# Optimization experiments

Hardware: AMD Instinct MI355X
Metric: run time of the kernel (lower is better)

Reference implementation:

```python
import jax, jax.numpy as jnp
import numpy as np

NUM_HEADS = 12
HEAD_SIZE = 64  # hidden 768 / 12 heads


def setup_inputs() -> dict:
    key = jax.random.key(0)
    ks = jax.random.split(key, 5)
    B, M, P, H = 8, 4, 512, 768
    scale = 1.0 / np.sqrt(H)
    return {
        "hidden_states": jax.random.normal(ks[0], (B, M, P, H), dtype=jnp.float32),
        "Wq": jax.random.normal(ks[1], (H, H), dtype=jnp.float32) * scale,
        "bq": jnp.zeros((H,), dtype=jnp.float32),
        "Wk": jax.random.normal(ks[2], (H, H), dtype=jnp.float32) * scale,
        "bk": jnp.zeros((H,), dtype=jnp.float32),
        "Wv": jax.random.normal(ks[3], (H, H), dtype=jnp.float32) * scale,
        "bv": jnp.zeros((H,), dtype=jnp.float32),
        "Wo": jax.random.normal(ks[4], (H, H), dtype=jnp.float32) * scale,
        "bo": jnp.zeros((H,), dtype=jnp.float32),
    }


def reference(hidden_states, Wq, bq, Wk, bk, Wv, bv, Wo, bo):
    # hidden_states: [B, M, P, H] (batch, modalities, patches, hidden)
    B, M, P, H = hidden_states.shape
    nh, hs = NUM_HEADS, HEAD_SIZE

    def split_heads(x):  # [B,M,P,H] -> [B,M,nh,P,hs]
        return x.reshape(B, M, P, nh, hs).transpose(0, 1, 3, 2, 4)

    q = split_heads(hidden_states @ Wq + bq)
    k = split_heads(hidden_states @ Wk + bk)
    v = split_heads(hidden_states @ Wv + bv)

    # per-modality, per-head attention over patches
    scores = jnp.einsum('bmnqh,bmnkh->bmnqk', q, k) / np.sqrt(hs).astype(jnp.float32)
    probs = jax.nn.softmax(scores, axis=-1)  # [B,M,nh,P,P]
    ctx = jnp.einsum('bmnqk,bmnkh->bmnqh', probs, v)
    ctx = ctx.transpose(0, 1, 3, 2, 4).reshape(B, M, P, H)  # merge heads

    # output projection (dropout rate 0.0 -> identity)
    return ctx @ Wo + bo
```

## Files before the change

kernel.cpp:

```cpp
#include <hip/hip_runtime.h>
#include <cstdint>
#include <cstddef>

#define H_DIM 768
#define NHEADS 12
#define HSZ 64
#define PATCH 512
#define MTOT 16384
#define SZT ((long)MTOT * H_DIM)

using short8 = __attribute__((ext_vector_type(8))) short;
using f32x4  = __attribute__((ext_vector_type(4))) float;
using us4    = __attribute__((ext_vector_type(4))) unsigned short;

#define GLL16(gp, lp) __builtin_amdgcn_global_load_lds( \
    (const __attribute__((address_space(1))) void*)(gp), \
    (__attribute__((address_space(3))) void*)(lp), 16, 0, 0)

__device__ __forceinline__ void split_f32(float x, unsigned short& h, unsigned short& l) {
    unsigned u = __float_as_uint(x);
    h = (unsigned short)(u >> 16);
    float rem = __uint_as_float(u & 0xffff0000u);
    float r = x - rem;
    unsigned v = __float_as_uint(r);
    v += 0x7fff + ((v >> 16) & 1);
    l = (unsigned short)(v >> 16);
}

__device__ __forceinline__ unsigned short bf16rne(float x) {
    unsigned v = __float_as_uint(x);
    v += 0x7fff + ((v >> 16) & 1);
    return (unsigned short)(v >> 16);
}

__global__ __launch_bounds__(256) void prep_x(const float* __restrict__ X,
                                              unsigned short* __restrict__ Xb)
{
    const long i = ((long)blockIdx.x * 256 + threadIdx.x) * 8;
    float4 a = *(const float4*)&X[i];
    float4 b = *(const float4*)&X[i + 4];
    float xs[8] = {a.x, a.y, a.z, a.w, b.x, b.y, b.z, b.w};
    us4 h0, h1;
    #pragma unroll
    for (int j = 0; j < 4; ++j) { h0[j] = bf16rne(xs[j]); h1[j] = bf16rne(xs[j + 4]); }
    *(us4*)&Xb[i] = h0; *(us4*)&Xb[i + 4] = h1;
}

template<int LO>
__global__ __launch_bounds__(256) void prep_w(const float* __restrict__ W,
                                              unsigned short* __restrict__ Whi,
                                              unsigned short* __restrict__ Wlo)
{
    __shared__ float T[64][65];
    const int kt = blockIdx.x * 64, nt = blockIdx.y * 64;
    const int tid = threadIdx.x;
    const int r = tid >> 2, c16 = (tid & 3) * 16;
    #pragma unroll
    for (int j = 0; j < 4; ++j) {
        float4 v = *(const float4*)&W[(long)(kt + r) * H_DIM + nt + c16 + j * 4];
        T[r][c16 + j*4 + 0] = v.x; T[r][c16 + j*4 + 1] = v.y;
        T[r][c16 + j*4 + 2] = v.z; T[r][c16 + j*4 + 3] = v.w;
    }
    __syncthreads();
    unsigned short* ph = &Whi[(long)(nt + r) * H_DIM + kt + c16];
    #pragma unroll
    for (int j = 0; j < 16; ++j) {
        if (LO) {
            unsigned short hh, ll;
            split_f32(T[c16 + j][r], hh, ll);
            ph[j] = hh;
            Wlo[(long)(nt + r) * H_DIM + kt + c16 + j] = ll;
        } else {
            ph[j] = bf16rne(T[c16 + j][r]);
        }
    }
}

__global__ __launch_bounds__(256, 4) void qkv_gemm(
    const unsigned short* __restrict__ Xb,
    const unsigned short* __restrict__ WqH, const unsigned short* __restrict__ WkH,
    const unsigned short* __restrict__ WvH,
    const float* __restrict__ bq, const float* __restrict__ bk, const float* __restrict__ bv,
    float qscale,
    unsigned short* __restrict__ Qt, unsigned short* __restrict__ Kp,
    unsigned short* __restrict__ Vp)
{
    __shared__ unsigned short As[8192];
    __shared__ unsigned short Bs[8192];

    const int s   = blockIdx.x + 18 * blockIdx.y;
    const int lid = (s & 7) * 288 + (s >> 3);
    const int bx  = lid % 18;
    const int by  = lid / 18;

    const int mat = bx / 6;
    const int n0  = (bx % 6) * 128;
    const int m0  = by * 128;
    const unsigned short* Bh = (mat == 0) ? WqH : (mat == 1) ? WkH : WvH;
    const float* bias        = (mat == 0) ? bq  : (mat == 1) ? bk  : bv;
    const float scale        = (mat == 0) ? qscale : 1.0f;

    const int tid  = threadIdx.x;
    const int lane = tid & 63;
    const int wv   = tid >> 6;
    const int wr   = wv >> 1, wc = wv & 1;
    const int q    = lane >> 4, l15 = lane & 15;

    const int srow   = tid >> 3;
    const int schunk = (tid & 7) ^ (srow & 7);

    char* ldsA = (char*)(&As[0]) + (wv << 10);
    char* ldsB = (char*)(&Bs[0]) + (wv << 10);

    f32x4 acc[4][4];
    #pragma unroll
    for (int i = 0; i < 4; ++i)
        #pragma unroll
        for (int j = 0; j < 4; ++j) acc[i][j] = 0;

    const int swz = (l15 & 7);

    for (int k0 = 0; k0 < H_DIM; k0 += 64) {
        #pragma unroll
        for (int i = 0; i < 4; ++i) {
            GLL16(Xb + (long)(m0 + i * 32 + srow) * H_DIM + k0 + schunk * 8,
                  ldsA + i * 4096);
            GLL16(Bh + (long)(n0 + i * 32 + srow) * H_DIM + k0 + schunk * 8,
                  ldsB + i * 4096);
        }
        __syncthreads();

        #pragma unroll
        for (int ks = 0; ks < 2; ++ks) {
            const int pc = ((ks * 4 + q) ^ swz) * 8;
            short8 ah[4], bh[4];
            #pragma unroll
            for (int t = 0; t < 4; ++t) {
                const int mr = wr * 64 + t * 16 + l15;
                ah[t] = *(const short8*)&As[mr * 64 + pc];
                const int nr = wc * 64 + t * 16 + l15;
                bh[t] = *(const short8*)&Bs[nr * 64 + pc];
            }
            #pragma unroll
            for (int mt = 0; mt < 4; ++mt)
                #pragma unroll
                for (int nt = 0; nt < 4; ++nt)
                    acc[mt][nt] = __builtin_amdgcn_mfma_f32_16x16x32_bf16(ah[mt], bh[nt], acc[mt][nt], 0, 0, 0);
        }
        __syncthreads();
    }

    #pragma unroll
    for (int nt = 0; nt < 4; ++nt) {
        const int col = n0 + wc * 64 + nt * 16 + l15;
        const float bcol = bias[col];
        const int h = col >> 6, d = col & 63;
        #pragma unroll
        for (int mt = 0; mt < 4; ++mt) {
            const int rowB = m0 + wr * 64 + mt * 16 + q * 4;
            #pragma unroll
            for (int r = 0; r < 4; ++r) {
                const int row = rowB + r;
                const float val = (acc[mt][nt][r] + bcol) * scale;
                const int bm = row >> 9, p = row & 511;
                const int bmh = bm * NHEADS + h;
                if (mat == 0) {
                    const long idx = ((long)bmh * 8 + (p >> 6)) * 4096 + (long)(p & 63) * 64 + d;
                    Qt[idx] = bf16rne(val);
                } else if (mat == 1) {
                    Kp[(long)bmh * 32768 + (long)p * 64 + d] = bf16rne(val);
                } else {
                    Vp[(long)bmh * 32768 + (long)d * 512 + p] = bf16rne(val);
                }
            }
        }
    }
}

__global__ __launch_bounds__(256, 4) void attn2(
    const unsigned short* __restrict__ Qt,
    const unsigned short* __restrict__ Kp, const unsigned short* __restrict__ Vp,
    unsigned short* __restrict__ Ctx)
{
    __shared__ unsigned short Ks[4096];
    __shared__ unsigned short Vs[4096];
    __shared__ unsigned short Ps[128 * 72];
    __shared__ float red[128][2];

    const int tid  = threadIdx.x;
    const int lane = tid & 63;
    const int wv   = tid >> 6;
    const int wr   = wv >> 1, wc = wv & 1;
    const int q    = lane >> 4, l15 = lane & 15;

    const int s   = blockIdx.x + 4 * blockIdx.y;
    const int lid = (s & 7) * 192 + (s >> 3);
    const int qt2 = lid & 3;
    const int bmh = lid >> 2;

    short8 qh[4][2];
    const long qtile = ((long)bmh * 8 + qt2 * 2 + wr) * 4096;
    #pragma unroll
    for (int mt = 0; mt < 4; ++mt)
        #pragma unroll
        for (int ks = 0; ks < 2; ++ks)
            qh[mt][ks] = *(const short8*)&Qt[qtile + (mt * 16 + l15) * 64 + ks * 32 + q * 8];

    f32x4 ctx[4][2];
    float l_cur[4][4];
    #pragma unroll
    for (int mt = 0; mt < 4; ++mt) {
        ctx[mt][0] = 0; ctx[mt][1] = 0;
        #pragma unroll
        for (int r = 0; r < 4; ++r) l_cur[mt][r] = 0.0f;
    }

    const long khead = (long)bmh * 32768;
    const int srow   = tid >> 3;
    const int gchunk = ((tid & 7) ^ (srow & 7)) * 8;
    char* dK = (char*)&Ks[0] + (wv << 10);
    char* dV = (char*)&Vs[0] + (wv << 10);

    for (int kt = 0; kt < 8; ++kt) {
        __syncthreads();
        {
            const long kb = khead + (long)kt * 64 * 64;
            GLL16(Kp + kb + (long)srow * 64 + gchunk,        dK);
            GLL16(Kp + kb + (long)(srow + 32) * 64 + gchunk, dK + 4096);
            const long vb = khead + (long)kt * 64;
            GLL16(Vp + vb + (long)srow * 512 + gchunk,        dV);
            GLL16(Vp + vb + (long)(srow + 32) * 512 + gchunk, dV + 4096);
        }
        __syncthreads();

        f32x4 s[4][2];
        #pragma unroll
        for (int mt = 0; mt < 4; ++mt) { s[mt][0] = 0; s[mt][1] = 0; }
        short8 kf[2][2];
        #pragma unroll
        for (int nt = 0; nt < 2; ++nt)
            #pragma unroll
            for (int ks = 0; ks < 2; ++ks) {
                const int key = wc * 32 + nt * 16 + l15;
                const int phys = (q + ks * 4) ^ (key & 7);
                kf[nt][ks] = *(const short8*)&Ks[key * 64 + phys * 8];
            }
        #pragma unroll
        for (int mt = 0; mt < 4; ++mt)
            #pragma unroll
            for (int nt = 0; nt < 2; ++nt)
                #pragma unroll
                for (int ks = 0; ks < 2; ++ks)
                    s[mt][nt] = __builtin_amdgcn_mfma_f32_16x16x32_bf16(qh[mt][ks], kf[nt][ks], s[mt][nt], 0, 0, 0);

        #pragma unroll
        for (int mt = 0; mt < 4; ++mt)
            #pragma unroll
            for (int r = 0; r < 4; ++r) {
                const int row = wr * 64 + mt * 16 + q * 4 + r;
                const float p0 = __builtin_amdgcn_exp2f(s[mt][0][r]);
                const float p1 = __builtin_amdgcn_exp2f(s[mt][1][r]);
                l_cur[mt][r] += p0 + p1;
                Ps[row * 72 + wc * 32 + l15]      = bf16rne(p0);
                Ps[row * 72 + wc * 32 + 16 + l15] = bf16rne(p1);
            }
        __syncthreads();

        short8 pf[4][2], vf[2][2];
        #pragma unroll
        for (int mt = 0; mt < 4; ++mt)
            #pragma unroll
            for (int ks = 0; ks < 2; ++ks)
                pf[mt][ks] = *(const short8*)&Ps[(wr * 64 + mt * 16 + l15) * 72 + ks * 32 + q * 8];
        #pragma unroll
        for (int nt = 0; nt < 2; ++nt)
            #pragma unroll
            for (int ks = 0; ks < 2; ++ks) {
                const int d = wc * 32 + nt * 16 + l15;
                const int phys = (q + ks * 4) ^ (d & 7);
                vf[nt][ks] = *(const short8*)&Vs[d * 64 + phys * 8];
            }
        #pragma unroll
        for (int mt = 0; mt < 4; ++mt)
            #pragma unroll
            for (int nt = 0; nt < 2; ++nt)
                #pragma unroll
                for (int ks = 0; ks < 2; ++ks)
                    ctx[mt][nt] = __builtin_amdgcn_mfma_f32_16x16x32_bf16(pf[mt][ks], vf[nt][ks], ctx[mt][nt], 0, 0, 0);
    }

    #pragma unroll
    for (int mt = 0; mt < 4; ++mt)
        #pragma unroll
        for (int r = 0; r < 4; ++r) {
            float v = l_cur[mt][r];
            v += __shfl_xor(v, 1);
            v += __shfl_xor(v, 2);
            v += __shfl_xor(v, 4);
            v += __shfl_xor(v, 8);
            if (l15 == 0) red[wr * 64 + mt * 16 + q * 4 + r][wc] = v;
        }
    __syncthreads();
    #pragma unroll
    for (int mt = 0; mt < 4; ++mt)
        #pragma unroll
        for (int r = 0; r < 4; ++r) {
            const int row = wr * 64 + mt * 16 + q * 4 + r;
            const float2 rd = *(const float2*)&red[row][0];
            const float inv = 1.0f / (rd.x + rd.y);
            const int trow = mt * 16 + q * 4 + r;
            #pragma unroll
            for (int nt = 0; nt < 2; ++nt) {
                const int col = wc * 32 + nt * 16 + l15;
                Ctx[qtile + trow * 64 + col] = bf16rne(ctx[mt][nt][r] * inv);
            }
        }
}

__global__ __launch_bounds__(256, 3) void oproj(
    const unsigned short* __restrict__ Ctx,
    const unsigned short* __restrict__ WoH, const unsigned short* __restrict__ WoL,
    const float* __restrict__ bo, float* __restrict__ out)
{
    __shared__ unsigned short As[8192];
    __shared__ unsigned short Bs[2][8192];

    const int tid  = threadIdx.x;
    const int lane = tid & 63;
    const int wv   = tid >> 6;
    const int wr   = wv >> 1, wc = wv & 1;
    const int q    = lane >> 4, l15 = lane & 15;

    const int s   = blockIdx.x + 6 * blockIdx.y;
    const int lid = (s & 7) * 96 + (s >> 3);
    const int n0  = (lid % 6) * 128;
    const int m0  = (lid / 6) * 128;

    const int srow   = tid >> 3;
    const int schunk = (tid & 7) ^ (srow & 7);

    char* ldsA = (char*)(&As[0]) + (wv << 10);
    char* ldsB = (char*)(&Bs[0][0]) + (wv << 10);

    f32x4 acc[4][4];
    #pragma unroll
    for (int i = 0; i < 4; ++i)
        #pragma unroll
        for (int j = 0; j < 4; ++j) acc[i][j] = 0;

    const int swz = (l15 & 7);

    for (int k0 = 0; k0 < H_DIM; k0 += 64) {
        const int h = k0 >> 6;
        #pragma unroll
        for (int i = 0; i < 4; ++i) {
            const int tok = m0 + i * 32 + srow;
            const long tile = ((long)(tok >> 9) * NHEADS + h) * 8 + ((tok >> 6) & 7);
            GLL16(Ctx + tile * 4096 + (long)(tok & 63) * 64 + schunk * 8, ldsA + i * 4096);
            GLL16(WoH + (long)(n0 + i * 32 + srow) * H_DIM + k0 + schunk * 8, ldsB + i * 4096);
            GLL16(WoL + (long)(n0 + i * 32 + srow) * H_DIM + k0 + schunk * 8, ldsB + 16384 + i * 4096);
        }
        __syncthreads();

        #pragma unroll
        for (int ks = 0; ks < 2; ++ks) {
            const int pc = ((ks * 4 + q) ^ swz) * 8;
            short8 ah[4], bh[4], bl[4];
            #pragma unroll
            for (int t = 0; t < 4; ++t) {
                const int mr = wr * 64 + t * 16 + l15;
                ah[t] = *(const short8*)&As[mr * 64 + pc];
                const int nr = wc * 64 + t * 16 + l15;
                bh[t] = *(const short8*)&Bs[0][nr * 64 + pc];
                bl[t] = *(const short8*)&Bs[1][nr * 64 + pc];
            }
            #pragma unroll
            for (int mt = 0; mt < 4; ++mt)
                #pragma unroll
                for (int nt = 0; nt < 4; ++nt) {
                    acc[mt][nt] = __builtin_amdgcn_mfma_f32_16x16x32_bf16(ah[mt], bh[nt], acc[mt][nt], 0, 0, 0);
                    acc[mt][nt] = __builtin_amdgcn_mfma_f32_16x16x32_bf16(ah[mt], bl[nt], acc[mt][nt], 0, 0, 0);
                }
        }
        __syncthreads();
    }

    #pragma unroll
    for (int nt = 0; nt < 4; ++nt) {
        const int col = n0 + wc * 64 + nt * 16 + l15;
        const float bcol = bo[col];
        #pragma unroll
        for (int mt = 0; mt < 4; ++mt) {
            const int rowB = m0 + wr * 64 + mt * 16 + q * 4;
            #pragma unroll
            for (int r = 0; r < 4; ++r)
                out[(long)(rowB + r) * H_DIM + col] = acc[mt][nt][r] + bcol;
        }
    }
}

extern "C" void kernel_launch(void* const* d_in, const int* in_sizes, int n_in,
                              void* d_out, int out_size, void* d_ws, size_t ws_size,
                              hipStream_t stream) {
    const float* X  = (const float*)d_in[0];
    const float* Wq = (const float*)d_in[1]; const float* bq = (const float*)d_in[2];
    const float* Wk = (const float*)d_in[3]; const float* bk = (const float*)d_in[4];
    const float* Wv = (const float*)d_in[5]; const float* bv = (const float*)d_in[6];
    const float* Wo = (const float*)d_in[7]; const float* bo = (const float*)d_in[8];

    unsigned short* wsu = (unsigned short*)d_ws;
    unsigned short* Qt  = wsu;
    unsigned short* Kp  = Qt + 12582912L;
    unsigned short* Vp  = Kp + 12582912L;
    unsigned short* Wt  = Vp + 12582912L;
    const long WP = (long)H_DIM * H_DIM;
    unsigned short* WqH = Wt;
    unsigned short* WkH = Wt + WP;
    unsigned short* WvH = Wt + 2 * WP;
    unsigned short* WoH = Wt + 3 * WP;
    unsigned short* WoL = Wt + 4 * WP;

    unsigned short* Xb = (unsigned short*)d_out;

    prep_x<<<(int)(SZT / 2048), 256, 0, stream>>>(X, Xb);
    dim3 wgrid(12, 12);
    prep_w<0><<<wgrid, 256, 0, stream>>>(Wq, WqH, nullptr);
    prep_w<0><<<wgrid, 256, 0, stream>>>(Wk, WkH, nullptr);
    prep_w<0><<<wgrid, 256, 0, stream>>>(Wv, WvH, nullptr);
    prep_w<1><<<wgrid, 256, 0, stream>>>(Wo, WoH, WoL);

    const float qscale = 0.125f * 1.4426950408889634f;
    qkv_gemm<<<dim3(18, 128), 256, 0, stream>>>(Xb, WqH, WkH, WvH,
                                                bq, bk, bv, qscale, Qt, Kp, Vp);

    attn2<<<dim3(4, 384), 256, 0, stream>>>(Qt, Kp, Vp, Qt);

    oproj<<<dim3(6, 128), 256, 0, stream>>>(Qt, WoH, WoL, bo, (float*)d_out);
}
```

Before: 313.7 us.

## Double-buffer K/V tiles in attention and fuse prep kernels into one launch

The attention kernel now keeps two LDS buffers for K and V and issues the global-to-LDS loads for the next key tile before computing on the current one. Explicit waitcnt and s_barrier calls replace __syncthreads so the prefetch can overlap the MFMA and softmax work. Occupancy is lowered to 3 blocks because of the larger LDS footprint. Separately, the five X and weight conversion kernels are merged into a single launch to cut launch overhead.

```diff
diff --git a/kernel.cpp b/kernel.cpp
--- a/kernel.cpp
+++ b/kernel.cpp
@@ -16,6 +16,8 @@
 #define GLL16(gp, lp) __builtin_amdgcn_global_load_lds( \
     (const __attribute__((address_space(1))) void*)(gp), \
     (__attribute__((address_space(3))) void*)(lp), 16, 0, 0)
+
+#define SB0() __builtin_amdgcn_sched_barrier(0)
 
 __device__ __forceinline__ void split_f32(float x, unsigned short& h, unsigned short& l) {
     unsigned u = __float_as_uint(x);
@@ -33,27 +35,38 @@
     return (unsigned short)(v >> 16);
 }
 
-__global__ __launch_bounds__(256) void prep_x(const float* __restrict__ X,
-                                              unsigned short* __restrict__ Xb)
-{
-    const long i = ((long)blockIdx.x * 256 + threadIdx.x) * 8;
-    float4 a = *(const float4*)&X[i];
-    float4 b = *(const float4*)&X[i + 4];
-    float xs[8] = {a.x, a.y, a.z, a.w, b.x, b.y, b.z, b.w};
-    us4 h0, h1;
-    #pragma unroll
-    for (int j = 0; j < 4; ++j) { h0[j] = bf16rne(xs[j]); h1[j] = bf16rne(xs[j + 4]); }
-    *(us4*)&Xb[i] = h0; *(us4*)&Xb[i + 4] = h1;
-}
-
-template<int LO>
-__global__ __launch_bounds__(256) void prep_w(const float* __restrict__ W,
-                                              unsigned short* __restrict__ Whi,
-                                              unsigned short* __restrict__ Wlo)
+__global__ __launch_bounds__(256) void prep_all(
+    const float* __restrict__ X, unsigned short* __restrict__ Xb,
+    const float* __restrict__ Wq, const float* __restrict__ Wk,
+    const float* __restrict__ Wv, const float* __restrict__ Wo,
+    unsigned short* __restrict__ WqH, unsigned short* __restrict__ WkH,
+    unsigned short* __restrict__ WvH, unsigned short* __restrict__ WoH,
+    unsigned short* __restrict__ WoL)
 {
     __shared__ float T[64][65];
-    const int kt = blockIdx.x * 64, nt = blockIdx.y * 64;
+    const int b = blockIdx.x;
     const int tid = threadIdx.x;
+
+    if (b < 6144) {
+        const long i = ((long)b * 256 + tid) * 8;
+        float4 a = *(const float4*)&X[i];
+        float4 c = *(const float4*)&X[i + 4];
+        float xs[8] = {a.x, a.y, a.z, a.w, c.x, c.y, c.z, c.w};
+        us4 h0, h1;
+        #pragma unroll
+        for (int j = 0; j < 4; ++j) { h0[j] = bf16rne(xs[j]); h1[j] = bf16rne(xs[j + 4]); }
+        *(us4*)&Xb[i] = h0; *(us4*)&Xb[i + 4] = h1;
+        return;
+    }
+
+    const int w     = b - 6144;
+    const int which = w / 144;
+    const int t     = w % 144;
+    const int kt    = (t / 12) * 64, nt = (t % 12) * 64;
+    const float* W  = (which == 0) ? Wq : (which == 1) ? Wk : (which == 2) ? Wv : Wo;
+    unsigned short* Whi = (which == 0) ? WqH : (which == 1) ? WkH : (which == 2) ? WvH : WoH;
+    const bool lo   = (which == 3);
+
     const int r = tid >> 2, c16 = (tid & 3) * 16;
     #pragma unroll
     for (int j = 0; j < 4; ++j) {
@@ -65,11 +78,11 @@
     unsigned short* ph = &Whi[(long)(nt + r) * H_DIM + kt + c16];
     #pragma unroll
     for (int j = 0; j < 16; ++j) {
-        if (LO) {
+        if (lo) {
             unsigned short hh, ll;
             split_f32(T[c16 + j][r], hh, ll);
             ph[j] = hh;
-            Wlo[(long)(nt + r) * H_DIM + kt + c16 + j] = ll;
+            WoL[(long)(nt + r) * H_DIM + kt + c16 + j] = ll;
         } else {
             ph[j] = bf16rne(T[c16 + j][r]);
         }
@@ -177,13 +190,13 @@
     }
 }
 
-__global__ __launch_bounds__(256, 4) void attn2(
+__global__ __launch_bounds__(256, 3) void attn2(
     const unsigned short* __restrict__ Qt,
     const unsigned short* __restrict__ Kp, const unsigned short* __restrict__ Vp,
     unsigned short* __restrict__ Ctx)
 {
-    __shared__ unsigned short Ks[4096];
-    __shared__ unsigned short Vs[4096];
+    __shared__ unsigned short Ks[2][4096];
+    __shared__ unsigned short Vs[2][4096];
     __shared__ unsigned short Ps[128 * 72];
     __shared__ float red[128][2];
 
@@ -218,24 +231,38 @@
     const long khead = (long)bmh * 32768;
     const int srow   = tid >> 3;
     const int gchunk = ((tid & 7) ^ (srow & 7)) * 8;
-    char* dK = (char*)&Ks[0] + (wv << 10);
-    char* dV = (char*)&Vs[0] + (wv << 10);
-
+    char* dK = (char*)&Ks[0][0] + (wv << 10);
+    char* dV = (char*)&Vs[0][0] + (wv << 10);
+
+    #define STAGE_KV(kt_, bsel) do { \
+        const long kb_ = khead + (long)(kt_) * 64 * 64; \
+        GLL16(Kp + kb_ + (long)srow * 64 + gchunk,        dK + (bsel) * 8192); \
+        GLL16(Kp + kb_ + (long)(srow + 32) * 64 + gchunk, dK + (bsel) * 8192 + 4096); \
+        const long vb_ = khead + (long)(kt_) * 64; \
+        GLL16(Vp + vb_ + (long)srow * 512 + gchunk,        dV + (bsel) * 8192); \
+        GLL16(Vp + vb_ + (long)(srow + 32) * 512 + gchunk, dV + (bsel) * 8192 + 4096); \
+    } while (0)
+
+    STAGE_KV(0, 0);
+
+    #pragma unroll 1
     for (int kt = 0; kt < 8; ++kt) {
-        __syncthreads();
-        {
-            const long kb = khead + (long)kt * 64 * 64;
-            GLL16(Kp + kb + (long)srow * 64 + gchunk,        dK);
-            GLL16(Kp + kb + (long)(srow + 32) * 64 + gchunk, dK + 4096);
-            const long vb = khead + (long)kt * 64;
-            GLL16(Vp + vb + (long)srow * 512 + gchunk,        dV);
-            GLL16(Vp + vb + (long)(srow + 32) * 512 + gchunk, dV + 4096);
-        }
-        __syncthreads();
-
-        f32x4 s[4][2];
-        #pragma unroll
-        for (int mt = 0; mt < 4; ++mt) { s[mt][0] = 0; s[mt][1] = 0; }
+        const int cur = kt & 1;
+        asm volatile("s_waitcnt lgkmcnt(0)" ::: "memory");
+        SB0();
+        __builtin_amdgcn_s_barrier();
+        if (kt < 7) {
+            STAGE_KV(kt + 1, cur ^ 1);
+            asm volatile("s_waitcnt vmcnt(4)" ::: "memory");
+        } else {
+            asm volatile("s_waitcnt vmcnt(0)" ::: "memory");
+        }
+        SB0();
+        __builtin_amdgcn_s_barrier();
+
+        f32x4 sv[4][2];
+        #pragma unroll
+        for (int mt = 0; mt < 4; ++mt) { sv[mt][0] = 0; sv[mt][1] = 0; }
         short8 kf[2][2];
         #pragma unroll
         for (int nt = 0; nt < 2; ++nt)
@@ -243,7 +270,7 @@
             for (int ks = 0; ks < 2; ++ks) {
                 const int key = wc * 32 + nt * 16 + l15;
                 const int phys = (q + ks * 4) ^ (key & 7);
-                kf[nt][ks] = *(const short8*)&Ks[key * 64 + phys * 8];
+                kf[nt][ks] = *(const short8*)&Ks[cur][key * 64 + phys * 8];
             }
         #pragma unroll
         for (int mt = 0; mt < 4; ++mt)
@@ -251,20 +278,22 @@
             for (int nt = 0; nt < 2; ++nt)
                 #pragma unroll
                 for (int ks = 0; ks < 2; ++ks)
-                    s[mt][nt] = __builtin_amdgcn_mfma_f32_16x16x32_bf16(qh[mt][ks], kf[nt][ks], s[mt][nt], 0, 0, 0);
+                    sv[mt][nt] = __builtin_amdgcn_mfma_f32_16x16x32_bf16(qh[mt][ks], kf[nt][ks], sv[mt][nt], 0, 0, 0);
 
         #pragma unroll
         for (int mt = 0; mt < 4; ++mt)
             #pragma unroll
             for (int r = 0; r < 4; ++r) {
                 const int row = wr * 64 + mt * 16 + q * 4 + r;
-                const float p0 = __builtin_amdgcn_exp2f(s[mt][0][r]);
-                const float p1 = __builtin_amdgcn_exp2f(s[mt][1][r]);
+                const float p0 = __builtin_amdgcn_exp2f(sv[mt][0][r]);
+                const float p1 = __builtin_amdgcn_exp2f(sv[mt][1][r]);
                 l_cur[mt][r] += p0 + p1;
                 Ps[row * 72 + wc * 32 + l15]      = bf16rne(p0);
                 Ps[row * 72 + wc * 32 + 16 + l15] = bf16rne(p1);
             }
-        __syncthreads();
+        asm volatile("s_waitcnt lgkmcnt(0)" ::: "memory");
+        SB0();
+        __builtin_amdgcn_s_barrier();
 
         short8 pf[4][2], vf[2][2];
         #pragma unroll
@@ -278,7 +307,7 @@
             for (int ks = 0; ks < 2; ++ks) {
                 const int d = wc * 32 + nt * 16 + l15;
                 const int phys = (q + ks * 4) ^ (d & 7);
-                vf[nt][ks] = *(const short8*)&Vs[d * 64 + phys * 8];
+                vf[nt][ks] = *(const short8*)&Vs[cur][d * 64 + phys * 8];
             }
         #pragma unroll
         for (int mt = 0; mt < 4; ++mt)
@@ -288,6 +317,7 @@
                 for (int ks = 0; ks < 2; ++ks)
                     ctx[mt][nt] = __builtin_amdgcn_mfma_f32_16x16x32_bf16(pf[mt][ks], vf[nt][ks], ctx[mt][nt], 0, 0, 0);
     }
+    #undef STAGE_KV
 
     #pragma unroll
     for (int mt = 0; mt < 4; ++mt)
@@ -422,12 +452,8 @@
 
     unsigned short* Xb = (unsigned short*)d_out;
 
-    prep_x<<<(int)(SZT / 2048), 256, 0, stream>>>(X, Xb);
-    dim3 wgrid(12, 12);
-    prep_w<0><<<wgrid, 256, 0, stream>>>(Wq, WqH, nullptr);
-    prep_w<0><<<wgrid, 256, 0, stream>>>(Wk, WkH, nullptr);
-    prep_w<0><<<wgrid, 256, 0, stream>>>(Wv, WvH, nullptr);
-    prep_w<1><<<wgrid, 256, 0, stream>>>(Wo, WoH, WoL);
+    prep_all<<<6720, 256, 0, stream>>>(X, Xb, Wq, Wk, Wv, Wo,
+                                       WqH, WkH, WvH, WoH, WoL);
 
     const float qscale = 0.125f * 1.4426950408889634f;
     qkv_gemm<<<dim3(18, 128), 256, 0, stream>>>(Xb, WqH, WkH, WvH,
```

Result: no change. 310.8 us (-0.9%).
